# Kernel optimization log

Measured on AMD Instinct MI355X. Metric: run time of the kernel, lower is better.

The kernel has to match this reference:

```python
import jax, jax.numpy as jnp
import numpy as np

N_ENT = 50000   # num_entities
N_REL = 500     # num_relations (x_r has 2*N_REL rows incl. inverses)
N_EDGE = 600000
DIM = 128
BN_EPS = 1e-5


def setup_inputs() -> dict:
    key = jax.random.key(0)
    ks = jax.random.split(key, 12)
    scale = 1.0 / np.sqrt(DIM)  # ~xavier
    return {
        "x_e": jax.random.normal(ks[0], (N_ENT, DIM), jnp.float32),
        "x_r": jax.random.normal(ks[1], (2 * N_REL, DIM), jnp.float32),
        "w_loop": jax.random.normal(ks[2], (DIM, DIM), jnp.float32) * scale,
        "w_fwd": jax.random.normal(ks[3], (DIM, DIM), jnp.float32) * scale,
        "w_bwd": jax.random.normal(ks[4], (DIM, DIM), jnp.float32) * scale,
        "w_rel": jax.random.normal(ks[5], (DIM, DIM), jnp.float32) * scale,  # nn.Linear weight (out,in), no bias
        "self_loop": jax.random.normal(ks[6], (1, DIM), jnp.float32) * scale,
        "bias": jnp.zeros((DIM,), jnp.float32),
        "bn_gamma": jnp.ones((DIM,), jnp.float32),
        "bn_beta": jnp.zeros((DIM,), jnp.float32),
        "edge_index": jax.random.randint(ks[7], (2, N_EDGE), 0, N_ENT, dtype=jnp.int32),
        "edge_type": jax.random.randint(ks[8], (N_EDGE,), 0, N_REL, dtype=jnp.int32),
    }


def _edge_weight(src, tgt):
    # SymmetricEdgeWeighting: sqrt(1/freq(src) * 1/freq(tgt))
    ones = jnp.ones(src.shape, jnp.float32)
    deg_s = jax.ops.segment_sum(ones, src, num_segments=N_ENT)
    deg_t = jax.ops.segment_sum(ones, tgt, num_segments=N_ENT)
    return jax.lax.rsqrt(deg_s[src] * deg_t[tgt])  # (E,)


def _message(x_e, x_r, src, tgt, et, weight):
    # gather -> compose (subtraction) -> matmul -> edge-weight scale -> scatter-add
    m = (x_e[src] - x_r[et]) @ weight                 # (E, D_out)
    m = m * _edge_weight(src, tgt)[:, None]
    return jnp.zeros((x_e.shape[0], m.shape[1]), m.dtype).at[tgt].add(m)


def reference(x_e, x_r, w_loop, w_fwd, w_bwd, w_rel, self_loop, bias,
              bn_gamma, bn_beta, edge_index, edge_type):
    et2 = 2 * edge_type
    src, tgt = edge_index[0], edge_index[1]
    out = ((x_e - self_loop) @ w_loop
           + _message(x_e, x_r, src, tgt, et2, w_fwd)
           + _message(x_e, x_r, tgt, src, et2 + 1, w_bwd)) / 3.0
    out = out + bias
    # BatchNorm1d (training-mode batch statistics)
    mean = jnp.mean(out, axis=0)
    var = jnp.var(out, axis=0)
    out = (out - mean) * jax.lax.rsqrt(var + BN_EPS) * bn_gamma + bn_beta
    # activation = Identity
    x_r_new = x_r @ w_rel.T  # nn.Linear, no bias
    return out, x_r_new
```

## Files before the change

### kernel.cpp

```cpp
#include <hip/hip_runtime.h>

namespace {

constexpr int N_ENTITY = 50000;
constexpr int NR2      = 1000;
constexpr int NE       = 600000;
constexpr int D        = 128;
constexpr int BCAP     = 16384;
constexpr float BN_EPS = 1e-5f;

constexpr int NB_BIN   = (NE + 2047) / 2048;
constexpr int NB_PREP  = 89;
constexpr int NB_GEMM  = (N_ENTITY + 63) / 64;
constexpr int NB_XR    = NR2 / 8;

constexpr size_t OFF_YF   = 0;
constexpr size_t OFF_YB   = OFF_YF + 1600000;
constexpr size_t OFF_YL   = OFF_YB + 1600000;
constexpr size_t OFF_ZF   = OFF_YL + 3200000;
constexpr size_t OFF_ZB   = OFF_ZF + 32000;
constexpr size_t OFF_WPK  = OFF_ZB + 32000;
constexpr size_t OFF_WRT  = OFF_WPK + 24576;
constexpr size_t OFF_SLW  = OFF_WRT + 16384;
constexpr size_t OFF_DEG0 = OFF_SLW + 256;
constexpr size_t OFF_DEG1 = OFF_DEG0 + 50048;
constexpr size_t OFF_OFF0 = OFF_DEG1 + 50048;
constexpr size_t OFF_OFF1 = OFF_OFF0 + 50048;
constexpr size_t OFF_RDG0 = OFF_OFF1 + 50048;
constexpr size_t OFF_RDG1 = OFF_RDG0 + 50048;
constexpr size_t OFF_GCNT = OFF_RDG1 + 50048;
constexpr size_t OFF_BIN0 = OFF_GCNT + 128;
constexpr size_t OFF_BIN1 = OFF_BIN0 + 2097152;
constexpr size_t OFF_EL0  = OFF_BIN1 + 2097152;
constexpr size_t OFF_EL1  = OFF_EL0 + 1048576;
constexpr size_t OFF_PART = OFF_EL1 + 1048576;
constexpr size_t OFF_KSH  = OFF_PART + 65536;

}

typedef __attribute__((ext_vector_type(8))) short bf16x8;
typedef __attribute__((ext_vector_type(4))) float f32x4;
typedef __attribute__((ext_vector_type(2))) float f32x2;

__device__ inline unsigned f2bf(float x) {
  unsigned u = __float_as_uint(x);
  return (u + 0x7FFFu + ((u >> 16) & 1u)) >> 16;
}
__device__ inline unsigned pack2bf(float a, float b) { return f2bf(a) | (f2bf(b) << 16); }
__device__ inline float bflo(unsigned v) { return __uint_as_float(v << 16); }
__device__ inline float bfhi(unsigned v) { return __uint_as_float(v & 0xFFFF0000u); }

__global__ __launch_bounds__(256) void k_binprep(
    const int* __restrict__ esrc, const int* __restrict__ etgt,
    const int* __restrict__ etype, unsigned* __restrict__ gcnt,
    uint2* __restrict__ bin0, uint2* __restrict__ bin1,
    const float* __restrict__ wl, const float* __restrict__ wf,
    const float* __restrict__ wb, const float* __restrict__ wrel,
    const float* __restrict__ sl,
    unsigned* __restrict__ wpk, float* __restrict__ wrT, float* __restrict__ slw) {
  const int tid = threadIdx.x;
  if (blockIdx.x >= NB_BIN) {
    const int b = blockIdx.x - NB_BIN;
    if (b < 64) {
      int i = b * 256 + tid;
      wrT[(i & 127) * D + (i >> 7)] = wrel[i];
    } else if (b == 64) {
      if (tid < 128) {
        float a = 0.f;
        for (int k = 0; k < D; ++k) a = fmaf(sl[k], wl[k * D + tid], a);
        slw[tid] = a;
      }
    } else {
      int idx = (b - 65) * 256 + tid;
      int w = idx / 2048, rem = idx % 2048;
      int frag = rem / 64, l = rem % 64;
      int ct = frag >> 2, kf = frag & 3;
      const float* W = (w == 0) ? wl : (w == 1) ? wf : wb;
      int krow = kf * 32 + (l >> 4) * 8;
      int col = ct * 16 + (l & 15);
      unsigned base = (unsigned)(w * 8192 + (frag * 64 + l) * 4);
#pragma unroll
      for (int j = 0; j < 8; j += 2) {
        float a = W[(krow + j) * D + col];
        float bb = W[(krow + j + 1) * D + col];
        wpk[base + (j >> 1)] = pack2bf(a, bb);
      }
    }
    return;
  }
  __shared__ unsigned cnt[128], base[128];
  if (tid < 128) cnt[tid] = 0;
  __syncthreads();
  const int start = blockIdx.x * 2048;
  int sv[8], tv[8];
#pragma unroll
  for (int k = 0; k < 8; ++k) {
    int i = start + k * 256 + tid;
    if (i < NE) {
      sv[k] = esrc[i]; tv[k] = etgt[i];
      atomicAdd(&cnt[(unsigned)sv[k] >> 10], 1u);
      atomicAdd(&cnt[64 + ((unsigned)tv[k] >> 10)], 1u);
    } else {
      sv[k] = -1; tv[k] = -1;
    }
  }
  __syncthreads();
  if (tid < 128) {
    base[tid] = atomicAdd(&gcnt[tid], cnt[tid]);
    cnt[tid] = 0;
  }
  __syncthreads();
#pragma unroll
  for (int k = 0; k < 8; ++k) {
    int i = start + k * 256 + tid;
    if (i < NE) {
      int s = sv[k], t = tv[k], et = etype[i];
      unsigned b0 = (unsigned)s >> 10, b1 = (unsigned)t >> 10;
      unsigned r0 = atomicAdd(&cnt[b0], 1u);
      unsigned p0 = base[b0] + r0;
      if (p0 < (unsigned)BCAP)
        bin0[(size_t)b0 * BCAP + p0] =
            make_uint2(((unsigned)s << 16) | (unsigned)t, (unsigned)(2 * et + 1));
      unsigned r1 = atomicAdd(&cnt[64 + b1], 1u);
      unsigned p1 = base[64 + b1] + r1;
      if (p1 < (unsigned)BCAP)
        bin1[(size_t)b1 * BCAP + p1] =
            make_uint2(((unsigned)t << 16) | (unsigned)s, (unsigned)(2 * et));
    }
  }
}

__global__ __launch_bounds__(256) void k_phase2(
    const float* __restrict__ xe, const unsigned* __restrict__ wpk,
    const float* __restrict__ slw, unsigned* __restrict__ Yl,
    unsigned* __restrict__ Yf, unsigned* __restrict__ Yb,
    const uint2* __restrict__ bin0, const uint2* __restrict__ bin1,
    const unsigned* __restrict__ gcnt,
    unsigned* __restrict__ deg0, unsigned* __restrict__ deg1,
    unsigned* __restrict__ off0, unsigned* __restrict__ off1,
    float* __restrict__ rdeg0, float* __restrict__ rdeg1,
    unsigned* __restrict__ el0, unsigned* __restrict__ el1,
    const float* __restrict__ xr, const float* __restrict__ wf,
    const float* __restrict__ wb, const float* __restrict__ wrT,
    unsigned* __restrict__ Zf, unsigned* __restrict__ Zb, float* __restrict__ xrnew) {
  __shared__ float smem[64 * 140];
  const int tid = threadIdx.x;

  if (blockIdx.x < NB_GEMM) {
    const int wv = tid >> 6, l = tid & 63;
    const int tile = blockIdx.x * 64;
    const int arow = tile + wv * 16 + (l & 15);
    const int arc = (arow < N_ENTITY) ? arow : (N_ENTITY - 1);
    const int kbase = (l >> 4) * 8;
    bf16x8 a[4];
#pragma unroll
    for (int kf = 0; kf < 4; ++kf) {
      const float* src = xe + (size_t)arc * D + kf * 32 + kbase;
      float4 lo = *(const float4*)(src);
      float4 hi = *(const float4*)(src + 4);
      union { bf16x8 v; unsigned u[4]; } cv;
      cv.u[0] = pack2bf(lo.x, lo.y);
      cv.u[1] = pack2bf(lo.z, lo.w);
      cv.u[2] = pack2bf(hi.x, hi.y);
      cv.u[3] = pack2bf(hi.z, hi.w);
      a[kf] = cv.v;
    }
    for (int widx = 0; widx < 3; ++widx) {
      const unsigned* wbase = wpk + widx * 8192;
#pragma unroll
      for (int ct = 0; ct < 8; ++ct) {
        f32x4 acc = {0.f, 0.f, 0.f, 0.f};
#pragma unroll
        for (int kf = 0; kf < 4; ++kf) {
          const bf16x8 b = *(const bf16x8*)(wbase + ((ct * 4 + kf) * 64 + l) * 4);
          acc = __builtin_amdgcn_mfma_f32_16x16x32_bf16(a[kf], b, acc, 0, 0, 0);
        }
        const int rbase = wv * 16 + (l >> 4) * 4;
        const int cc = ct * 16 + (l & 15);
#pragma unroll
        for (int j = 0; j < 4; ++j) smem[(rbase + j) * 140 + cc] = acc[j];
      }
      __syncthreads();
      for (int f = tid; f < 64 * 32; f += 256) {
        int row = f >> 5, c4 = (f & 31) * 4;
        int g = tile + row;
        if (g < N_ENTITY) {
          float4 v = *(float4*)(smem + row * 140 + c4);
          if (widx == 0) {
            float4 s = *(const float4*)(slw + c4);
            uint2 p = make_uint2(pack2bf(v.x - s.x, v.y - s.y),
                                 pack2bf(v.z - s.z, v.w - s.w));
            *(uint2*)(Yl + (size_t)g * 64 + (c4 >> 1)) = p;
          } else {
            int p = __builtin_amdgcn_cvt_pk_fp8_f32(v.x, v.y, 0, false);
            p = __builtin_amdgcn_cvt_pk_fp8_f32(v.z, v.w, p, true);
            unsigned* dst = ((widx == 1) ? Yf : Yb);
            dst[(size_t)g * 32 + (c4 >> 2)] = (unsigned)p;
          }
        }
      }
      __syncthreads();
    }
    return;
  }

  if (blockIdx.x < NB_GEMM + 128) {
    unsigned* hist = (unsigned*)smem;
    unsigned* excl = hist + 1024;
    unsigned* wtot = excl + 1024;
    unsigned* wof  = wtot + 4;
    const int bb = (blockIdx.x - NB_GEMM) & 63, dd = (blockIdx.x - NB_GEMM) >> 6;
    const uint2* bin = dd ? bin1 : bin0;
    unsigned* deg = dd ? deg1 : deg0;
    unsigned* off = dd ? off1 : off0;
    float* rdeg = dd ? rdeg1 : rdeg0;
    unsigned* el = dd ? el1 : el0;
    const int n0 = bb << 10;
    unsigned m = gcnt[dd * 64 + bb];
    if (m > (unsigned)BCAP) m = (unsigned)BCAP;
    const uint2* src = bin + (size_t)bb * BCAP;

#pragma unroll
    for (int k = 0; k < 4; ++k) hist[tid * 4 + k] = 0;
    __syncthreads();
    for (unsigned j = tid; j < m; j += 256) {
      unsigned n = src[j].x >> 16;
      atomicAdd(&hist[n - n0], 1u);
    }
    __syncthreads();
    unsigned h0 = hist[tid * 4], h1 = hist[tid * 4 + 1];
    unsigned h2 = hist[tid * 4 + 2], h3 = hist[tid * 4 + 3];
    unsigned ts = h0 + h1 + h2 + h3;
    unsigned incl = ts;
    const int lane = tid & 63, wid = tid >> 6;
#pragma unroll
    for (int dsh = 1; dsh < 64; dsh <<= 1) {
      unsigned nv = __shfl_up(incl, dsh, 64);
      if (lane >= dsh) incl += nv;
    }
    if (lane == 63) wtot[wid] = incl;
    __syncthreads();
    if (tid == 0) {
      unsigned a = 0;
      for (int w = 0; w < 4; ++w) { wof[w] = a; a += wtot[w]; }
    }
    __syncthreads();
    unsigned ex = wof[wid] + incl - ts;
    excl[tid * 4] = ex;
    excl[tid * 4 + 1] = ex + h0;
    excl[tid * 4 + 2] = ex + h0 + h1;
    excl[tid * 4 + 3] = ex + h0 + h1 + h2;
    const unsigned bstart = (unsigned)bb * BCAP;
#pragma unroll
    for (int k = 0; k < 4; ++k) {
      int idx = tid * 4 + k;
      int n = n0 + idx;
      if (n < N_ENTITY) {
        unsigned dv = hist[idx];
        deg[n] = dv;
        off[n] = bstart + excl[idx];
        rdeg[n] = rsqrtf((float)dv);
      }
    }
    __syncthreads();
#pragma unroll
    for (int k = 0; k < 4; ++k) hist[tid * 4 + k] = 0;
    __syncthreads();
    for (unsigned j = tid; j < m; j += 256) {
      uint2 e = src[j];
      unsigned li = (e.x >> 16) - (unsigned)n0;
      unsigned other = e.x & 0xFFFFu;
      unsigned r = atomicAdd(&hist[li], 1u);
      el[bstart + excl[li] + r] = (other << 10) | e.y;
    }
    return;
  }

  float* xs = smem;
  const int tile = (blockIdx.x - NB_GEMM - 128) * 8;
  for (int f = tid * 4; f < 8 * 128; f += 1024) {
    int rr = f >> 7, kk = f & 127;
    *(float4*)(xs + rr * 132 + kk) = *(const float4*)(xr + (size_t)(tile + rr) * D + kk);
  }
  __syncthreads();
  const int c4 = (tid & 31) * 4;
  const int rs = tid >> 5;
  const int row = tile + rs;
  float4 af = make_float4(0, 0, 0, 0), ab = make_float4(0, 0, 0, 0), ar = make_float4(0, 0, 0, 0);
#pragma unroll 4
  for (int k = 0; k < 128; ++k) {
    float x = xs[rs * 132 + k];
    float4 f4 = *(const float4*)(wf + k * D + c4);
    float4 b4 = *(const float4*)(wb + k * D + c4);
    float4 r4 = *(const float4*)(wrT + k * D + c4);
    af.x = fmaf(x, f4.x, af.x); af.y = fmaf(x, f4.y, af.y);
    af.z = fmaf(x, f4.z, af.z); af.w = fmaf(x, f4.w, af.w);
    ab.x = fmaf(x, b4.x, ab.x); ab.y = fmaf(x, b4.y, ab.y);
    ab.z = fmaf(x, b4.z, ab.z); ab.w = fmaf(x, b4.w, ab.w);
    ar.x = fmaf(x, r4.x, ar.x); ar.y = fmaf(x, r4.y, ar.y);
    ar.z = fmaf(x, r4.z, ar.z); ar.w = fmaf(x, r4.w, ar.w);
  }
  int pf = __builtin_amdgcn_cvt_pk_fp8_f32(af.x, af.y, 0, false);
  pf = __builtin_amdgcn_cvt_pk_fp8_f32(af.z, af.w, pf, true);
  int pb = __builtin_amdgcn_cvt_pk_fp8_f32(ab.x, ab.y, 0, false);
  pb = __builtin_amdgcn_cvt_pk_fp8_f32(ab.z, ab.w, pb, true);
  Zf[(size_t)row * 32 + (c4 >> 2)] = (unsigned)pf;
  Zb[(size_t)row * 32 + (c4 >> 2)] = (unsigned)pb;
  *(float4*)(xrnew + (size_t)row * D + c4) = ar;
}

__device__ inline void pstep(const unsigned* __restrict__ Y, const unsigned* __restrict__ Z,
                             unsigned d, float rw, int i, int half, int col, float4& acc) {
  int e = i + half;
  unsigned pk = __shfl(d, e, 64);
  float w = __shfl(rw, e, 64);
  unsigned yv = Y[(size_t)(pk >> 10) * 32 + col];
  unsigned zv = Z[(size_t)(pk & 1023u) * 32 + col];
  f32x2 ylo = __builtin_amdgcn_cvt_pk_f32_fp8((int)yv, false);
  f32x2 yhi = __builtin_amdgcn_cvt_pk_f32_fp8((int)yv, true);
  f32x2 zlo = __builtin_amdgcn_cvt_pk_f32_fp8((int)zv, false);
  f32x2 zhi = __builtin_amdgcn_cvt_pk_f32_fp8((int)zv, true);
  acc.x = fmaf(w, ylo.x - zlo.x, acc.x);
  acc.y = fmaf(w, ylo.y - zlo.y, acc.y);
  acc.z = fmaf(w, yhi.x - zhi.x, acc.z);
  acc.w = fmaf(w, yhi.y - zhi.y, acc.w);
}

__global__ __launch_bounds__(256) void k_gather(
    const unsigned* __restrict__ Yl,
    const unsigned* __restrict__ Yf, const unsigned* __restrict__ Yb,
    const unsigned* __restrict__ Zf, const unsigned* __restrict__ Zb,
    const unsigned* __restrict__ deg0, const unsigned* __restrict__ deg1,
    const unsigned* __restrict__ off0, const unsigned* __restrict__ off1,
    const float* __restrict__ rdeg0, const float* __restrict__ rdeg1,
    const unsigned* __restrict__ el0, const unsigned* __restrict__ el1,
    float* __restrict__ out) {
  const int lane = threadIdx.x & 63;
  const int half = lane >> 5;
  const int col = lane & 31;
  const int n = (int)((blockIdx.x * blockDim.x + threadIdx.x) >> 6);
  if (n >= N_ENTITY) return;

  float4 accA, accB = make_float4(0.f, 0.f, 0.f, 0.f);
  if (half == 0) {
    uint2 lv = *(const uint2*)(Yl + (size_t)n * 64 + col * 2);
    accA = make_float4(bflo(lv.x), bfhi(lv.x), bflo(lv.y), bfhi(lv.y));
  } else {
    accA = make_float4(0.f, 0.f, 0.f, 0.f);
  }

  unsigned p0 = off0[n], c0t = deg0[n];
  unsigned p1 = off1[n], c1t = deg1[n];
  const float r0n = rdeg0[n], r1n = rdeg1[n];

  while (c0t > 0 || c1t > 0) {
    int c0 = (int)((c0t < 64u) ? c0t : 64u);
    int c1 = (int)((c1t < 64u) ? c1t : 64u);
    unsigned d0 = 0, d1 = 0;
    float rw0 = 0.f, rw1 = 0.f;
    if (lane < c0) {
      d0 = el0[p0 + lane];
      rw0 = r0n * rdeg1[d0 >> 10];
    }
    if (lane < c1) {
      d1 = el1[p1 + lane];
      rw1 = r1n * rdeg0[d1 >> 10];
    }
    int i0 = 0, i1 = 0;
    while (i0 + 4 <= c0 && i1 + 4 <= c1) {
      int ea0 = i0 + half, ea1 = i0 + 2 + half;
      int eb0 = i1 + half, eb1 = i1 + 2 + half;
      unsigned pka = __shfl(d0, ea0, 64); float wa = __shfl(rw0, ea0, 64);
      unsigned pkb = __shfl(d0, ea1, 64); float wb = __shfl(rw0, ea1, 64);
      unsigned pkc = __shfl(d1, eb0, 64); float wc = __shfl(rw1, eb0, 64);
      unsigned pkd = __shfl(d1, eb1, 64); float wd = __shfl(rw1, eb1, 64);
      unsigned ya = Yb[(size_t)(pka >> 10) * 32 + col];
      unsigned za = Zb[(size_t)(pka & 1023u) * 32 + col];
      unsigned yb = Yb[(size_t)(pkb >> 10) * 32 + col];
      unsigned zb = Zb[(size_t)(pkb & 1023u) * 32 + col];
      unsigned yc = Yf[(size_t)(pkc >> 10) * 32 + col];
      unsigned zc = Zf[(size_t)(pkc & 1023u) * 32 + col];
      unsigned yd = Yf[(size_t)(pkd >> 10) * 32 + col];
      unsigned zd = Zf[(size_t)(pkd & 1023u) * 32 + col];
      f32x2 al = __builtin_amdgcn_cvt_pk_f32_fp8((int)ya, false);
      f32x2 ah = __builtin_amdgcn_cvt_pk_f32_fp8((int)ya, true);
      f32x2 aul = __builtin_amdgcn_cvt_pk_f32_fp8((int)za, false);
      f32x2 auh = __builtin_amdgcn_cvt_pk_f32_fp8((int)za, true);
      f32x2 bl = __builtin_amdgcn_cvt_pk_f32_fp8((int)yb, false);
      f32x2 bh = __builtin_amdgcn_cvt_pk_f32_fp8((int)yb, true);
      f32x2 bul = __builtin_amdgcn_cvt_pk_f32_fp8((int)zb, false);
      f32x2 buh = __builtin_amdgcn_cvt_pk_f32_fp8((int)zb, true);
      f32x2 cl = __builtin_amdgcn_cvt_pk_f32_fp8((int)yc, false);
      f32x2 ch = __builtin_amdgcn_cvt_pk_f32_fp8((int)yc, true);
      f32x2 cul = __builtin_amdgcn_cvt_pk_f32_fp8((int)zc, false);
      f32x2 cuh = __builtin_amdgcn_cvt_pk_f32_fp8((int)zc, true);
      f32x2 dl = __builtin_amdgcn_cvt_pk_f32_fp8((int)yd, false);
      f32x2 dh = __builtin_amdgcn_cvt_pk_f32_fp8((int)yd, true);
      f32x2 dul = __builtin_amdgcn_cvt_pk_f32_fp8((int)zd, false);
      f32x2 duh = __builtin_amdgcn_cvt_pk_f32_fp8((int)zd, true);
      accA.x = fmaf(wa, al.x - aul.x, accA.x);
      accA.y = fmaf(wa, al.y - aul.y, accA.y);
      accA.z = fmaf(wa, ah.x - auh.x, accA.z);
      accA.w = fmaf(wa, ah.y - auh.y, accA.w);
      accB.x = fmaf(wb, bl.x - bul.x, accB.x);
      accB.y = fmaf(wb, bl.y - bul.y, accB.y);
      accB.z = fmaf(wb, bh.x - buh.x, accB.z);
      accB.w = fmaf(wb, bh.y - buh.y, accB.w);
      accA.x = fmaf(wc, cl.x - cul.x, accA.x);
      accA.y = fmaf(wc, cl.y - cul.y, accA.y);
      accA.z = fmaf(wc, ch.x - cuh.x, accA.z);
      accA.w = fmaf(wc, ch.y - cuh.y, accA.w);
      accB.x = fmaf(wd, dl.x - dul.x, accB.x);
      accB.y = fmaf(wd, dl.y - dul.y, accB.y);
      accB.z = fmaf(wd, dh.x - duh.x, accB.z);
      accB.w = fmaf(wd, dh.y - duh.y, accB.w);
      i0 += 4; i1 += 4;
    }
    for (; i0 < c0; i0 += 2) pstep(Yb, Zb, d0, rw0, i0, half, col, accA);
    for (; i1 < c1; i1 += 2) pstep(Yf, Zf, d1, rw1, i1, half, col, accB);
    p0 += (unsigned)c0; c0t -= (unsigned)c0;
    p1 += (unsigned)c1; c1t -= (unsigned)c1;
  }

  accA.x += accB.x; accA.y += accB.y; accA.z += accB.z; accA.w += accB.w;
  accA.x += __shfl_down(accA.x, 32, 64);
  accA.y += __shfl_down(accA.y, 32, 64);
  accA.z += __shfl_down(accA.z, 32, 64);
  accA.w += __shfl_down(accA.w, 32, 64);
  if (half == 0) *(float4*)(out + (size_t)n * D + col * 4) = accA;
}

__global__ void k_stats1(const float* __restrict__ out, float* __restrict__ part) {
  const int t = threadIdx.x;
  float s = 0.f, sq = 0.f;
  for (int r = blockIdx.x; r < N_ENTITY; r += gridDim.x) {
    float v = out[(size_t)r * D + t];
    s += v;
    sq = fmaf(v, v, sq);
  }
  part[blockIdx.x * 256 + t] = s;
  part[blockIdx.x * 256 + 128 + t] = sq;
}

__global__ void k_stats2(const float* __restrict__ part, const float* __restrict__ gamma,
                         const float* __restrict__ beta, float* __restrict__ ksh) {
  const int t = threadIdx.x;
  float s = 0.f, sq = 0.f;
  for (int b = 0; b < 256; ++b) {
    s += part[b * 256 + t];
    sq += part[b * 256 + 128 + t];
  }
  float mean = s * (1.f / N_ENTITY);
  float var = sq * (1.f / N_ENTITY) - mean * mean;
  float scale = gamma[t] * (1.f / 3.f) * rsqrtf(var * (1.f / 9.f) + BN_EPS);
  ksh[t] = scale;
  ksh[128 + t] = beta[t] - mean * scale;
}

__global__ void k_final(float* __restrict__ out, const float* __restrict__ ksh) {
  const size_t i4 = ((size_t)blockIdx.x * blockDim.x + threadIdx.x) * 4;
  if (i4 >= (size_t)N_ENTITY * D) return;
  const int c = (int)(i4 & 127);
  float4 v = *(float4*)(out + i4);
  v.x = fmaf(v.x, ksh[c + 0], ksh[128 + c + 0]);
  v.y = fmaf(v.y, ksh[c + 1], ksh[128 + c + 1]);
  v.z = fmaf(v.z, ksh[c + 2], ksh[128 + c + 2]);
  v.w = fmaf(v.w, ksh[c + 3], ksh[128 + c + 3]);
  *(float4*)(out + i4) = v;
}

extern "C" void kernel_launch(void* const* d_in, const int* in_sizes, int n_in,
                              void* d_out, int out_size, void* d_ws, size_t ws_size,
                              hipStream_t stream) {
  const float* xe    = (const float*)d_in[0];
  const float* xr    = (const float*)d_in[1];
  const float* wl    = (const float*)d_in[2];
  const float* wf    = (const float*)d_in[3];
  const float* wb    = (const float*)d_in[4];
  const float* wrel  = (const float*)d_in[5];
  const float* sl    = (const float*)d_in[6];
  const float* gamma = (const float*)d_in[8];
  const float* beta  = (const float*)d_in[9];
  const int* eidx    = (const int*)d_in[10];
  const int* etype   = (const int*)d_in[11];
  const int* esrc = eidx;
  const int* etgt = eidx + NE;

  float* outF  = (float*)d_out;
  float* xrnew = (float*)d_out + (size_t)N_ENTITY * D;

  float* wsf = (float*)d_ws;
  unsigned* wsu = (unsigned*)d_ws;
  unsigned* Yf  = wsu + OFF_YF;
  unsigned* Yb  = wsu + OFF_YB;
  unsigned* Yl  = wsu + OFF_YL;
  unsigned* Zf  = wsu + OFF_ZF;
  unsigned* Zb  = wsu + OFF_ZB;
  unsigned* wpk = wsu + OFF_WPK;
  float* wrT = wsf + OFF_WRT;
  float* slw = wsf + OFF_SLW;
  unsigned* deg0 = wsu + OFF_DEG0;
  unsigned* deg1 = wsu + OFF_DEG1;
  unsigned* off0 = wsu + OFF_OFF0;
  unsigned* off1 = wsu + OFF_OFF1;
  float* rdeg0 = wsf + OFF_RDG0;
  float* rdeg1 = wsf + OFF_RDG1;
  unsigned* gcnt = wsu + OFF_GCNT;
  uint2* bin0 = (uint2*)(wsu + OFF_BIN0);
  uint2* bin1 = (uint2*)(wsu + OFF_BIN1);
  unsigned* el0 = wsu + OFF_EL0;
  unsigned* el1 = wsu + OFF_EL1;
  float* part = wsf + OFF_PART;
  float* ksh  = wsf + OFF_KSH;

  hipMemsetAsync(gcnt, 0, 128 * sizeof(unsigned), stream);

  k_binprep<<<NB_BIN + NB_PREP, 256, 0, stream>>>(
      esrc, etgt, etype, gcnt, bin0, bin1, wl, wf, wb, wrel, sl, wpk, wrT, slw);

  k_phase2<<<NB_GEMM + 128 + NB_XR, 256, 0, stream>>>(
      xe, wpk, slw, Yl, Yf, Yb,
      bin0, bin1, gcnt, deg0, deg1, off0, off1, rdeg0, rdeg1, el0, el1,
      xr, wf, wb, wrT, Zf, Zb, xrnew);

  k_gather<<<(N_ENTITY * 64 + 255) / 256, 256, 0, stream>>>(
      Yl, Yf, Yb, Zf, Zb, deg0, deg1, off0, off1, rdeg0, rdeg1, el0, el1, outF);

  k_stats1<<<256, 128, 0, stream>>>(outF, part);
  k_stats2<<<1, 128, 0, stream>>>(part, gamma, beta, ksh);
  k_final<<<(N_ENTITY * D / 4 + 255) / 256, 256, 0, stream>>>(outF, ksh);
}
```

Baseline: 185.7 us.

## Reschedule edge binning to overlap entity GEMM and split bucketing kernel

Moves edge binning out of the weight-prep kernel and into the same launch as the entity GEMM and relation GEMM blocks, so binning runs alongside the dense work instead of ahead of it. The per-bucket CSR construction becomes its own kernel launched afterwards, and weight prep becomes a small standalone kernel. Each binning block now handles 4096 edges instead of 2048, which halves the number of global counter atomics. The cost is one extra kernel launch, and the 128 bucketing blocks no longer overlap with the GEMM.

```diff
diff --git a/kernel.cpp b/kernel.cpp
--- a/kernel.cpp
+++ b/kernel.cpp
@@ -9,7 +9,7 @@
 constexpr int BCAP     = 16384;
 constexpr float BN_EPS = 1e-5f;
 
-constexpr int NB_BIN   = (NE + 2047) / 2048;
+constexpr int NB_BIN   = (NE + 4095) / 4096;
 constexpr int NB_PREP  = 89;
 constexpr int NB_GEMM  = (N_ENTITY + 63) / 64;
 constexpr int NB_XR    = NR2 / 8;
@@ -50,105 +50,101 @@
 __device__ inline float bflo(unsigned v) { return __uint_as_float(v << 16); }
 __device__ inline float bfhi(unsigned v) { return __uint_as_float(v & 0xFFFF0000u); }
 
-__global__ __launch_bounds__(256) void k_binprep(
-    const int* __restrict__ esrc, const int* __restrict__ etgt,
-    const int* __restrict__ etype, unsigned* __restrict__ gcnt,
-    uint2* __restrict__ bin0, uint2* __restrict__ bin1,
+__global__ __launch_bounds__(256) void k_prep(
     const float* __restrict__ wl, const float* __restrict__ wf,
     const float* __restrict__ wb, const float* __restrict__ wrel,
     const float* __restrict__ sl,
     unsigned* __restrict__ wpk, float* __restrict__ wrT, float* __restrict__ slw) {
-  const int tid = threadIdx.x;
-  if (blockIdx.x >= NB_BIN) {
-    const int b = blockIdx.x - NB_BIN;
-    if (b < 64) {
-      int i = b * 256 + tid;
-      wrT[(i & 127) * D + (i >> 7)] = wrel[i];
-    } else if (b == 64) {
-      if (tid < 128) {
-        float a = 0.f;
-        for (int k = 0; k < D; ++k) a = fmaf(sl[k], wl[k * D + tid], a);
-        slw[tid] = a;
-      }
-    } else {
-      int idx = (b - 65) * 256 + tid;
-      int w = idx / 2048, rem = idx % 2048;
-      int frag = rem / 64, l = rem % 64;
-      int ct = frag >> 2, kf = frag & 3;
-      const float* W = (w == 0) ? wl : (w == 1) ? wf : wb;
-      int krow = kf * 32 + (l >> 4) * 8;
-      int col = ct * 16 + (l & 15);
-      unsigned base = (unsigned)(w * 8192 + (frag * 64 + l) * 4);
-#pragma unroll
-      for (int j = 0; j < 8; j += 2) {
-        float a = W[(krow + j) * D + col];
-        float bb = W[(krow + j + 1) * D + col];
-        wpk[base + (j >> 1)] = pack2bf(a, bb);
-      }
-    }
-    return;
-  }
-  __shared__ unsigned cnt[128], base[128];
-  if (tid < 128) cnt[tid] = 0;
-  __syncthreads();
-  const int start = blockIdx.x * 2048;
-  int sv[8], tv[8];
-#pragma unroll
-  for (int k = 0; k < 8; ++k) {
-    int i = start + k * 256 + tid;
-    if (i < NE) {
-      sv[k] = esrc[i]; tv[k] = etgt[i];
-      atomicAdd(&cnt[(unsigned)sv[k] >> 10], 1u);
-      atomicAdd(&cnt[64 + ((unsigned)tv[k] >> 10)], 1u);
-    } else {
-      sv[k] = -1; tv[k] = -1;
-    }
-  }
-  __syncthreads();
-  if (tid < 128) {
-    base[tid] = atomicAdd(&gcnt[tid], cnt[tid]);
-    cnt[tid] = 0;
-  }
-  __syncthreads();
-#pragma unroll
-  for (int k = 0; k < 8; ++k) {
-    int i = start + k * 256 + tid;
-    if (i < NE) {
-      int s = sv[k], t = tv[k], et = etype[i];
-      unsigned b0 = (unsigned)s >> 10, b1 = (unsigned)t >> 10;
-      unsigned r0 = atomicAdd(&cnt[b0], 1u);
-      unsigned p0 = base[b0] + r0;
-      if (p0 < (unsigned)BCAP)
-        bin0[(size_t)b0 * BCAP + p0] =
-            make_uint2(((unsigned)s << 16) | (unsigned)t, (unsigned)(2 * et + 1));
-      unsigned r1 = atomicAdd(&cnt[64 + b1], 1u);
-      unsigned p1 = base[64 + b1] + r1;
-      if (p1 < (unsigned)BCAP)
-        bin1[(size_t)b1 * BCAP + p1] =
-            make_uint2(((unsigned)t << 16) | (unsigned)s, (unsigned)(2 * et));
-    }
-  }
-}
-
-__global__ __launch_bounds__(256) void k_phase2(
+  const int b = blockIdx.x;
+  const int t = threadIdx.x;
+  if (b < 64) {
+    int i = b * 256 + t;
+    wrT[(i & 127) * D + (i >> 7)] = wrel[i];
+  } else if (b == 64) {
+    if (t < 128) {
+      float a = 0.f;
+      for (int k = 0; k < D; ++k) a = fmaf(sl[k], wl[k * D + t], a);
+      slw[t] = a;
+    }
+  } else {
+    int idx = (b - 65) * 256 + t;
+    int w = idx / 2048, rem = idx % 2048;
+    int frag = rem / 64, l = rem % 64;
+    int ct = frag >> 2, kf = frag & 3;
+    const float* W = (w == 0) ? wl : (w == 1) ? wf : wb;
+    int krow = kf * 32 + (l >> 4) * 8;
+    int col = ct * 16 + (l & 15);
+    unsigned base = (unsigned)(w * 8192 + (frag * 64 + l) * 4);
+#pragma unroll
+    for (int j = 0; j < 8; j += 2) {
+      float a = W[(krow + j) * D + col];
+      float bb = W[(krow + j + 1) * D + col];
+      wpk[base + (j >> 1)] = pack2bf(a, bb);
+    }
+  }
+}
+
+__global__ __launch_bounds__(256) void k_mid(
+    const int* __restrict__ esrc, const int* __restrict__ etgt,
+    const int* __restrict__ etype, unsigned* __restrict__ gcnt,
+    uint2* __restrict__ bin0, uint2* __restrict__ bin1,
     const float* __restrict__ xe, const unsigned* __restrict__ wpk,
     const float* __restrict__ slw, unsigned* __restrict__ Yl,
     unsigned* __restrict__ Yf, unsigned* __restrict__ Yb,
-    const uint2* __restrict__ bin0, const uint2* __restrict__ bin1,
-    const unsigned* __restrict__ gcnt,
-    unsigned* __restrict__ deg0, unsigned* __restrict__ deg1,
-    unsigned* __restrict__ off0, unsigned* __restrict__ off1,
-    float* __restrict__ rdeg0, float* __restrict__ rdeg1,
-    unsigned* __restrict__ el0, unsigned* __restrict__ el1,
     const float* __restrict__ xr, const float* __restrict__ wf,
     const float* __restrict__ wb, const float* __restrict__ wrT,
     unsigned* __restrict__ Zf, unsigned* __restrict__ Zb, float* __restrict__ xrnew) {
   __shared__ float smem[64 * 140];
   const int tid = threadIdx.x;
 
-  if (blockIdx.x < NB_GEMM) {
+  if (blockIdx.x < NB_BIN) {
+    unsigned* cnt  = (unsigned*)smem;
+    unsigned* base = cnt + 128;
+    if (tid < 128) cnt[tid] = 0;
+    __syncthreads();
+    const int start = blockIdx.x * 4096;
+    int sv[16], tv[16];
+#pragma unroll
+    for (int k = 0; k < 16; ++k) {
+      int i = start + k * 256 + tid;
+      if (i < NE) {
+        sv[k] = esrc[i]; tv[k] = etgt[i];
+        atomicAdd(&cnt[(unsigned)sv[k] >> 10], 1u);
+        atomicAdd(&cnt[64 + ((unsigned)tv[k] >> 10)], 1u);
+      } else {
+        sv[k] = -1; tv[k] = -1;
+      }
+    }
+    __syncthreads();
+    if (tid < 128) {
+      base[tid] = atomicAdd(&gcnt[tid], cnt[tid]);
+      cnt[tid] = 0;
+    }
+    __syncthreads();
+#pragma unroll
+    for (int k = 0; k < 16; ++k) {
+      int i = start + k * 256 + tid;
+      if (i < NE) {
+        int s = sv[k], t = tv[k], et = etype[i];
+        unsigned b0 = (unsigned)s >> 10, b1 = (unsigned)t >> 10;
+        unsigned r0 = atomicAdd(&cnt[b0], 1u);
+        unsigned p0 = base[b0] + r0;
+        if (p0 < (unsigned)BCAP)
+          bin0[(size_t)b0 * BCAP + p0] =
+              make_uint2(((unsigned)s << 16) | (unsigned)t, (unsigned)(2 * et + 1));
+        unsigned r1 = atomicAdd(&cnt[64 + b1], 1u);
+        unsigned p1 = base[64 + b1] + r1;
+        if (p1 < (unsigned)BCAP)
+          bin1[(size_t)b1 * BCAP + p1] =
+              make_uint2(((unsigned)t << 16) | (unsigned)s, (unsigned)(2 * et));
+      }
+    }
+    return;
+  }
+
+  if (blockIdx.x < NB_BIN + NB_GEMM) {
     const int wv = tid >> 6, l = tid & 63;
-    const int tile = blockIdx.x * 64;
+    const int tile = (blockIdx.x - NB_BIN) * 64;
     const int arow = tile + wv * 16 + (l & 15);
     const int arc = (arow < N_ENTITY) ? arow : (N_ENTITY - 1);
     const int kbase = (l >> 4) * 8;
@@ -204,80 +200,8 @@
     return;
   }
 
-  if (blockIdx.x < NB_GEMM + 128) {
-    unsigned* hist = (unsigned*)smem;
-    unsigned* excl = hist + 1024;
-    unsigned* wtot = excl + 1024;
-    unsigned* wof  = wtot + 4;
-    const int bb = (blockIdx.x - NB_GEMM) & 63, dd = (blockIdx.x - NB_GEMM) >> 6;
-    const uint2* bin = dd ? bin1 : bin0;
-    unsigned* deg = dd ? deg1 : deg0;
-    unsigned* off = dd ? off1 : off0;
-    float* rdeg = dd ? rdeg1 : rdeg0;
-    unsigned* el = dd ? el1 : el0;
-    const int n0 = bb << 10;
-    unsigned m = gcnt[dd * 64 + bb];
-    if (m > (unsigned)BCAP) m = (unsigned)BCAP;
-    const uint2* src = bin + (size_t)bb * BCAP;
-
-#pragma unroll
-    for (int k = 0; k < 4; ++k) hist[tid * 4 + k] = 0;
-    __syncthreads();
-    for (unsigned j = tid; j < m; j += 256) {
-      unsigned n = src[j].x >> 16;
-      atomicAdd(&hist[n - n0], 1u);
-    }
-    __syncthreads();
-    unsigned h0 = hist[tid * 4], h1 = hist[tid * 4 + 1];
-    unsigned h2 = hist[tid * 4 + 2], h3 = hist[tid * 4 + 3];
-    unsigned ts = h0 + h1 + h2 + h3;
-    unsigned incl = ts;
-    const int lane = tid & 63, wid = tid >> 6;
-#pragma unroll
-    for (int dsh = 1; dsh < 64; dsh <<= 1) {
-      unsigned nv = __shfl_up(incl, dsh, 64);
-      if (lane >= dsh) incl += nv;
-    }
-    if (lane == 63) wtot[wid] = incl;
-    __syncthreads();
-    if (tid == 0) {
-      unsigned a = 0;
-      for (int w = 0; w < 4; ++w) { wof[w] = a; a += wtot[w]; }
-    }
-    __syncthreads();
-    unsigned ex = wof[wid] + incl - ts;
-    excl[tid * 4] = ex;
-    excl[tid * 4 + 1] = ex + h0;
-    excl[tid * 4 + 2] = ex + h0 + h1;
-    excl[tid * 4 + 3] = ex + h0 + h1 + h2;
-    const unsigned bstart = (unsigned)bb * BCAP;
-#pragma unroll
-    for (int k = 0; k < 4; ++k) {
-      int idx = tid * 4 + k;
-      int n = n0 + idx;
-      if (n < N_ENTITY) {
-        unsigned dv = hist[idx];
-        deg[n] = dv;
-        off[n] = bstart + excl[idx];
-        rdeg[n] = rsqrtf((float)dv);
-      }
-    }
-    __syncthreads();
-#pragma unroll
-    for (int k = 0; k < 4; ++k) hist[tid * 4 + k] = 0;
-    __syncthreads();
-    for (unsigned j = tid; j < m; j += 256) {
-      uint2 e = src[j];
-      unsigned li = (e.x >> 16) - (unsigned)n0;
-      unsigned other = e.x & 0xFFFFu;
-      unsigned r = atomicAdd(&hist[li], 1u);
-      el[bstart + excl[li] + r] = (other << 10) | e.y;
-    }
-    return;
-  }
-
   float* xs = smem;
-  const int tile = (blockIdx.x - NB_GEMM - 128) * 8;
+  const int tile = (blockIdx.x - NB_BIN - NB_GEMM) * 8;
   for (int f = tid * 4; f < 8 * 128; f += 1024) {
     int rr = f >> 7, kk = f & 127;
     *(float4*)(xs + rr * 132 + kk) = *(const float4*)(xr + (size_t)(tile + rr) * D + kk);
@@ -307,6 +231,82 @@
   Zf[(size_t)row * 32 + (c4 >> 2)] = (unsigned)pf;
   Zb[(size_t)row * 32 + (c4 >> 2)] = (unsigned)pb;
   *(float4*)(xrnew + (size_t)row * D + c4) = ar;
+}
+
+__global__ __launch_bounds__(256) void k_bucket(
+    const uint2* __restrict__ bin0, const uint2* __restrict__ bin1,
+    const unsigned* __restrict__ gcnt,
+    unsigned* __restrict__ deg0, unsigned* __restrict__ deg1,
+    unsigned* __restrict__ off0, unsigned* __restrict__ off1,
+    float* __restrict__ rdeg0, float* __restrict__ rdeg1,
+    unsigned* __restrict__ el0, unsigned* __restrict__ el1) {
+  __shared__ unsigned hist[1024], excl[1024];
+  __shared__ unsigned wtot[4], wof[4];
+  const int tid = threadIdx.x;
+  const int bb = blockIdx.x & 63, dd = blockIdx.x >> 6;
+  const uint2* bin = dd ? bin1 : bin0;
+  unsigned* deg = dd ? deg1 : deg0;
+  unsigned* off = dd ? off1 : off0;
+  float* rdeg = dd ? rdeg1 : rdeg0;
+  unsigned* el = dd ? el1 : el0;
+  const int n0 = bb << 10;
+  unsigned m = gcnt[dd * 64 + bb];
+  if (m > (unsigned)BCAP) m = (unsigned)BCAP;
+  const uint2* src = bin + (size_t)bb * BCAP;
+
+#pragma unroll
+  for (int k = 0; k < 4; ++k) hist[tid * 4 + k] = 0;
+  __syncthreads();
+  for (unsigned j = tid; j < m; j += 256) {
+    unsigned n = src[j].x >> 16;
+    atomicAdd(&hist[n - n0], 1u);
+  }
+  __syncthreads();
+  unsigned h0 = hist[tid * 4], h1 = hist[tid * 4 + 1];
+  unsigned h2 = hist[tid * 4 + 2], h3 = hist[tid * 4 + 3];
+  unsigned ts = h0 + h1 + h2 + h3;
+  unsigned incl = ts;
+  const int lane = tid & 63, wid = tid >> 6;
+#pragma unroll
+  for (int dsh = 1; dsh < 64; dsh <<= 1) {
+    unsigned nv = __shfl_up(incl, dsh, 64);
+    if (lane >= dsh) incl += nv;
+  }
+  if (lane == 63) wtot[wid] = incl;
+  __syncthreads();
+  if (tid == 0) {
+    unsigned a = 0;
+    for (int w = 0; w < 4; ++w) { wof[w] = a; a += wtot[w]; }
+  }
+  __syncthreads();
+  unsigned ex = wof[wid] + incl - ts;
+  excl[tid * 4] = ex;
+  excl[tid * 4 + 1] = ex + h0;
+  excl[tid * 4 + 2] = ex + h0 + h1;
+  excl[tid * 4 + 3] = ex + h0 + h1 + h2;
+  const unsigned bstart = (unsigned)bb * BCAP;
+#pragma unroll
+  for (int k = 0; k < 4; ++k) {
+    int idx = tid * 4 + k;
+    int n = n0 + idx;
+    if (n < N_ENTITY) {
+      unsigned dv = hist[idx];
+      deg[n] = dv;
+      off[n] = bstart + excl[idx];
+      rdeg[n] = rsqrtf((float)dv);
+    }
+  }
+  __syncthreads();
+#pragma unroll
+  for (int k = 0; k < 4; ++k) hist[tid * 4 + k] = 0;
+  __syncthreads();
+  for (unsigned j = tid; j < m; j += 256) {
+    uint2 e = src[j];
+    unsigned li = (e.x >> 16) - (unsigned)n0;
+    unsigned other = e.x & 0xFFFFu;
+    unsigned r = atomicAdd(&hist[li], 1u);
+    el[bstart + excl[li] + r] = (other << 10) | e.y;
+  }
 }
 
 __device__ inline void pstep(const unsigned* __restrict__ Y, const unsigned* __restrict__ Z,
@@ -515,13 +515,15 @@
 
   hipMemsetAsync(gcnt, 0, 128 * sizeof(unsigned), stream);
 
-  k_binprep<<<NB_BIN + NB_PREP, 256, 0, stream>>>(
-      esrc, etgt, etype, gcnt, bin0, bin1, wl, wf, wb, wrel, sl, wpk, wrT, slw);
-
-  k_phase2<<<NB_GEMM + 128 + NB_XR, 256, 0, stream>>>(
+  k_prep<<<NB_PREP, 256, 0, stream>>>(wl, wf, wb, wrel, sl, wpk, wrT, slw);
+
+  k_mid<<<NB_BIN + NB_GEMM + NB_XR, 256, 0, stream>>>(
+      esrc, etgt, etype, gcnt, bin0, bin1,
       xe, wpk, slw, Yl, Yf, Yb,
-      bin0, bin1, gcnt, deg0, deg1, off0, off1, rdeg0, rdeg1, el0, el1,
       xr, wf, wb, wrT, Zf, Zb, xrnew);
+
+  k_bucket<<<128, 256, 0, stream>>>(bin0, bin1, gcnt, deg0, deg1, off0, off1,
+                                    rdeg0, rdeg1, el0, el1);
 
   k_gather<<<(N_ENTITY * 64 + 255) / 256, 256, 0, stream>>>(
       Yl, Yf, Yb, Zf, Zb, deg0, deg1, off0, off1, rdeg0, rdeg1, el0, el1, outF);
```

After: 203.1 us. +9.3%, slower.
